# Kernel tuning notes

Measured on AMD Instinct MI355X. Metric: run time of the kernel, lower is better.

The kernel has to match this reference:

```python
import jax, jax.numpy as jnp
import numpy as np

L = 13   # num hidden states (embeddings + 12 layers)
B = 32   # batch
N = 512  # sequence length
H = 768  # per-layer hidden size
M = 384  # mapping_size = embed_size // downsample_D_factor
E = 768  # embed_size


def setup_inputs() -> dict:
    key = jax.random.key(0)
    ks = jax.random.split(key, 8)
    s = 0.02
    return {
        "all_hidden_features": jax.random.normal(ks[0], (L, B, N, H), jnp.float32),
        "lengths": jax.random.randint(ks[1], (B,), 1, N + 1),  # valid lengths in [1, N]
        "W_down": jax.random.normal(ks[2], (L, H, M), jnp.float32) * s,
        "b_down": jnp.zeros((L, M), jnp.float32),
        "g_down": jnp.ones((L, M), jnp.float32),
        "beta_down": jnp.zeros((L, M), jnp.float32),
        "W_proj": jax.random.normal(ks[3], (M, M), jnp.float32) * s,
        "b_proj": jnp.zeros((M,), jnp.float32),
        "g_proj": jnp.ones((M,), jnp.float32),
        "beta_proj": jnp.zeros((M,), jnp.float32),
        "W_up": jax.random.normal(ks[4], (M, E), jnp.float32) * s,
        "b_up": jnp.zeros((E,), jnp.float32),
        "W_gate": jax.random.normal(ks[5], (M, 1), jnp.float32) * s,
        "b_gate": jnp.zeros((1,), jnp.float32),
    }


def _ln(x, g, b, eps=1e-5):
    mu = jnp.mean(x, axis=-1, keepdims=True)
    var = jnp.var(x, axis=-1, keepdims=True)
    return (x - mu) * jax.lax.rsqrt(var + eps) * g + b


def reference(all_hidden_features, lengths, W_down, b_down, g_down, beta_down,
              W_proj, b_proj, g_proj, beta_proj, W_up, b_up, W_gate, b_gate):
    # mask: [B, N] 1.0 for valid positions
    mask = (jnp.arange(N)[None, :] < lengths[:, None]).astype(jnp.float32)

    # per-layer downsample: Linear + LayerNorm over all L layers at once -> [L, B, N, M]
    down = _ln(jnp.einsum('lbnh,lhm->lbnm', all_hidden_features, W_down)
               + b_down[:, None, None, :],
               g_down[:, None, None, :], beta_down[:, None, None, :])

    anchor_feat = down[-1]                      # [B, N, M]
    denom = jnp.sum(mask, axis=1)[:, None]      # [B, 1]
    anchor = jnp.sum(anchor_feat * mask[:, :, None], axis=1) / denom  # [B, M]

    targets = down[:-1]                         # [L-1, B, N, M]
    t_agg = jnp.sum(targets * mask[None, :, :, None], axis=2) / denom[None]  # [L-1, B, M]

    # cross-attention: relu + L1-normalized weights + identity, mask on context dim
    cw = jnp.einsum('bnm,lbkm->lbnk', anchor_feat, targets)  # [L-1, B, N, N]
    cw = jax.nn.relu(cw * mask[None, :, None, :])
    cw = cw / (jnp.sum(cw, axis=-1, keepdims=True) + 1e-8) + jnp.eye(N, dtype=cw.dtype)
    merged = jnp.einsum('lbnk,lbkm->lbnm', cw, targets)      # [L-1, B, N, M]

    # gated fusion across layers
    logits = (jnp.einsum('lbm,mo->lbo', anchor[None] * t_agg, W_gate) + b_gate)[..., 0]  # [L-1, B]
    conf = jax.nn.softmax(logits.T, axis=1)                  # [B, L-1]
    msum = jnp.einsum('lbnm,bl->bnm', merged, conf)          # [B, N, M]

    out = anchor_feat + _ln(msum @ W_proj + b_proj, g_proj, beta_proj)
    return (jax.nn.relu(out) @ W_up + b_up, lengths)
```

## Files before the change

kernel.cpp:

```cpp
#include <hip/hip_runtime.h>

#define LL 13
#define BB 32
#define NN 512
#define HH 768
#define MM 384
#define EE 768
#define BN (BB*NN)
#define K12 (12*NN)

typedef __attribute__((ext_vector_type(8))) short s16x8;
typedef __attribute__((ext_vector_type(4))) float f32x4;
typedef __attribute__((ext_vector_type(4))) unsigned int u32x4;
typedef unsigned int u32;
#define AS1 __attribute__((address_space(1)))
#define AS3 __attribute__((address_space(3)))

__device__ __forceinline__ u32 cvtpk2(float a, float b) {
    u32 r; asm("v_cvt_pk_bf16_f32 %0, %1, %2" : "=v"(r) : "v"(a), "v"(b));
    return r;
}
__device__ __forceinline__ short f2bf_hw(float f) {
    u32 r; asm("v_cvt_pk_bf16_f32 %0, %1, %2" : "=v"(r) : "v"(f), "v"(f));
    return (short)r;
}
__device__ __forceinline__ float bf2f(short h) {
    union { u32 u; float f; } c; c.u = ((u32)(unsigned short)h) << 16;
    return c.f;
}
__device__ __forceinline__ void gload16(const void* g, void* l) {
    __builtin_amdgcn_global_load_lds((const AS1 u32*)g, (AS3 u32*)l, 16, 0, 0);
}

template<int AM>
__device__ __forceinline__ void gemm_core(const char* At, const char* At2, int lda,
                                          const char* Bt, int ldb,
                                          int K, char* lds, f32x4 acc[4][4])
{
    const int tid  = threadIdx.x;
    const int lane = tid & 63;
    const int w    = tid >> 6;
    const int mt0 = (w >> 1) * 4;
    const int nt0 = (w & 1) * 4;

    const int rg0 = (w*2)*16 + (lane & 15);
    const int rg1 = rg0 + 16;
    const int kcb = (lane >> 4) * 16;
    const char* gb0 = Bt + (size_t)rg0 * ldb * 2 + kcb;
    const char* gb1 = Bt + (size_t)rg1 * ldb * 2 + kcb;
    const int lboff0 = 8192 + (w*2)*1024;
    const int lboff1 = lboff0 + 1024;

    auto mfma_step = [&](int bo) {
        s16x8 af[4], bf4[4];
        char* sA = lds + bo;
        char* sB = sA + 8192;
        #pragma unroll
        for (int i = 0; i < 4; ++i) af[i] = *(const s16x8*)(sA + ((mt0+i)<<10) + lane*16);
        #pragma unroll
        for (int j = 0; j < 4; ++j) bf4[j] = *(const s16x8*)(sB + ((nt0+j)<<10) + lane*16);
        #pragma unroll
        for (int i = 0; i < 4; ++i)
            #pragma unroll
            for (int j = 0; j < 4; ++j)
                acc[i][j] = __builtin_amdgcn_mfma_f32_16x16x32_bf16(af[i], bf4[j], acc[i][j], 0, 0, 0);
    };

    if (AM == 0) {
        const char* ga0 = At + (size_t)rg0 * lda * 2 + kcb;
        const char* ga1 = At + (size_t)rg1 * lda * 2 + kcb;
        const int laoff0 = (w*2)*1024, laoff1 = laoff0 + 1024;
        gload16(ga0, lds + laoff0); gload16(ga1, lds + laoff1);
        gload16(gb0, lds + lboff0); gload16(gb1, lds + lboff1);
        ga0 += 64; ga1 += 64; gb0 += 64; gb1 += 64;
        __syncthreads();
        int bo = 0;
        for (int k0 = 32; k0 < K; k0 += 32) {
            const int nbo = bo ^ 16384;
            gload16(ga0, lds + nbo + laoff0); gload16(ga1, lds + nbo + laoff1);
            gload16(gb0, lds + nbo + lboff0); gload16(gb1, lds + nbo + lboff1);
            ga0 += 64; ga1 += 64; gb0 += 64; gb1 += 64;
            mfma_step(bo);
            __syncthreads();
            bo = nbo;
        }
        mfma_step(bo);
    } else {
        size_t goff_[4]; int loff_[4];
        #pragma unroll
        for (int c = 0; c < 4; ++c) {
            int id = c*256 + tid;
            int row = id >> 3, c16 = id & 7;
            goff_[c] = (size_t)row * lda * 4 + c16 * 16;
            loff_[c] = ((row>>4)*64 + (row&15) + (c16>>1)*16)*16 + (c16&1)*8;
        }
        f32x4 g[4];
        #pragma unroll
        for (int c = 0; c < 4; ++c) {
            g[c] = *(const f32x4*)(At + goff_[c]);
            if (AM == 2) {
                f32x4 h = *(const f32x4*)(At2 + goff_[c]);
                g[c][0]+=h[0]; g[c][1]+=h[1]; g[c][2]+=h[2]; g[c][3]+=h[3];
            }
        }
        gload16(gb0, lds + lboff0); gload16(gb1, lds + lboff1);
        gb0 += 64; gb1 += 64;
        #pragma unroll
        for (int c = 0; c < 4; ++c) {
            u32* d = (u32*)(lds + loff_[c]);
            d[0] = cvtpk2(g[c][0], g[c][1]);
            d[1] = cvtpk2(g[c][2], g[c][3]);
        }
        __syncthreads();
        int bo = 0;
        size_t kb = 128;
        for (int k0 = 32; k0 < K; k0 += 32, kb += 128) {
            const int nbo = bo ^ 16384;
            #pragma unroll
            for (int c = 0; c < 4; ++c) {
                g[c] = *(const f32x4*)(At + goff_[c] + kb);
                if (AM == 2) {
                    f32x4 h = *(const f32x4*)(At2 + goff_[c] + kb);
                    g[c][0]+=h[0]; g[c][1]+=h[1]; g[c][2]+=h[2]; g[c][3]+=h[3];
                }
            }
            gload16(gb0, lds + nbo + lboff0); gload16(gb1, lds + nbo + lboff1);
            gb0 += 64; gb1 += 64;
            mfma_step(bo);
            #pragma unroll
            for (int c = 0; c < 4; ++c) {
                u32* d = (u32*)(lds + nbo + loff_[c]);
                d[0] = cvtpk2(g[c][0], g[c][1]);
                d[1] = cvtpk2(g[c][2], g[c][3]);
            }
            __syncthreads();
            bo = nbo;
        }
        mfma_step(bo);
    }
}

__device__ __forceinline__ void zero_acc(f32x4 acc[4][4]) {
    #pragma unroll
    for (int i = 0; i < 4; ++i)
        #pragma unroll
        for (int j = 0; j < 4; ++j) {
            acc[i][j][0] = 0.f; acc[i][j][1] = 0.f;
            acc[i][j][2] = 0.f; acc[i][j][3] = 0.f;
        }
}

__global__ __launch_bounds__(256) void k_zero(float* __restrict__ p, int n4)
{
    int i = blockIdx.x*256 + threadIdx.x;
    if (i < n4) { f32x4 z = {0.f,0.f,0.f,0.f}; ((f32x4*)p)[i] = z; }
}

__global__ __launch_bounds__(256) void k_wt(const float* __restrict__ in, short* __restrict__ out,
                                            int R, int C, size_t zin, size_t zout)
{
    __shared__ short L[64][80];
    const float* I = in + (size_t)blockIdx.z * zin;
    short* O = out + (size_t)blockIdx.z * zout;
    const int r0 = blockIdx.y * 64, c0 = blockIdx.x * 64;
    const int t = threadIdx.x;
    {
        int r = t >> 2, cq = (t & 3) * 16;
        const float* p = I + (size_t)(r0 + r) * C + c0 + cq;
        f32x4 u0 = *(const f32x4*)(p);
        f32x4 u1 = *(const f32x4*)(p + 4);
        f32x4 u2 = *(const f32x4*)(p + 8);
        f32x4 u3 = *(const f32x4*)(p + 12);
        u32x4 pa, pb;
        pa[0]=cvtpk2(u0[0],u0[1]); pa[1]=cvtpk2(u0[2],u0[3]);
        pa[2]=cvtpk2(u1[0],u1[1]); pa[3]=cvtpk2(u1[2],u1[3]);
        pb[0]=cvtpk2(u2[0],u2[1]); pb[1]=cvtpk2(u2[2],u2[3]);
        pb[2]=cvtpk2(u3[0],u3[1]); pb[3]=cvtpk2(u3[2],u3[3]);
        *(u32x4*)&L[r][cq]     = pa;
        *(u32x4*)&L[r][cq + 8] = pb;
    }
    __syncthreads();
    #pragma unroll
    for (int it = 0; it < 2; ++it) {
        int id = it * 256 + t;
        int cc = id >> 3, rq = id & 7;
        s16x8 v;
        #pragma unroll
        for (int e = 0; e < 8; ++e) v[e] = L[rq*8 + e][cc];
        *(s16x8*)(O + (size_t)(c0 + cc) * R + r0 + rq*8) = v;
    }
}

__global__ __launch_bounds__(256) void k_down(const float* __restrict__ X,
                                              const short* __restrict__ WdT,
                                              const float* __restrict__ bd,
                                              short* __restrict__ down)
{
    __shared__ char lds[36864];
    const int lg = ((blockIdx.x & 7) * 624) + (blockIdx.x >> 3);
    const int col0 = (lg % 3) * 128;
    const int row0 = ((lg / 3) & 127) * 128;
    const int l = lg / 384;
    const char* At = (const char*)(X   + (size_t)l*BN*HH + (size_t)row0*HH);
    const char* Bt = (const char*)(WdT + (size_t)l*MM*HH + (size_t)col0*HH);
    f32x4 acc[4][4]; zero_acc(acc);
    gemm_core<1>(At, nullptr, HH, Bt, HH, HH, lds, acc);

    const int tid = threadIdx.x, lane = tid & 63, w = tid >> 6;
    const int wr = w >> 1, wc = w & 1;
    float bj[4];
    #pragma unroll
    for (int j = 0; j < 4; ++j) bj[j] = bd[l*MM + col0 + wc*64 + j*16 + (lane & 15)];
    __syncthreads();
    short* ep = (short*)(lds + w * 9216);
    #pragma unroll
    for (int i = 0; i < 4; ++i) {
        int rr = i*16 + (lane >> 4) * 4;
        #pragma unroll
        for (int j = 0; j < 4; ++j) {
            int cc = j*16 + (lane & 15);
            #pragma unroll
            for (int r = 0; r < 4; ++r)
                ep[(rr + r)*72 + cc] = f2bf_hw(acc[i][j][r] + bj[j]);
        }
    }
    __syncthreads();
    short* C = down + (size_t)l*BN*MM;
    #pragma unroll
    for (int it = 0; it < 8; ++it) {
        int c = it*64 + lane;
        int row = c >> 3, kq = c & 7;
        s16x8 v = *(const s16x8*)(ep + row*72 + kq*8);
        int grow = row0 + wr*64 + row;
        int gcol = col0 + wc*64 + kq*8;
        *(s16x8*)(C + (size_t)grow*MM + gcol) = v;
    }
}

__global__ __launch_bounds__(256) void k_ln(short* __restrict__ down,
                                            const float* __restrict__ g,
                                            const float* __restrict__ beta,
                                            short* __restrict__ downTb,
                                            const int* __restrict__ lengths,
                                            float* __restrict__ t_raw,
                                            float* __restrict__ a_raw)
{
    __shared__ short Lt[64][392];
    __shared__ float sacc[4][384];
    const int blk = blockIdx.x;
    const int l = blk / (BB*8);
    const int rem = blk % (BB*8);
    const int b = rem >> 3;
    const int n0 = (rem & 7) * 64;
    const int tid = threadIdx.x, lane = tid & 63, w = tid >> 6;
    const int len = lengths[b];
    float racc[6] = {0.f,0.f,0.f,0.f,0.f,0.f};

    for (int it = 0; it < 16; ++it) {
        int ri = it*4 + w;
        int n = n0 + ri;
        short* p = down + (((size_t)l*BB + b)*NN + n) * MM;
        u32* pu = (u32*)p;
        float f[6]; float s = 0.f, s2 = 0.f;
        #pragma unroll
        for (int t = 0; t < 3; ++t) {
            u32 q = pu[lane + t*64];
            float lo = bf2f((short)(q & 0xffff));
            float hi = bf2f((short)(q >> 16));
            f[2*t] = lo; f[2*t+1] = hi;
            s += lo + hi; s2 += lo*lo + hi*hi;
        }
        #pragma unroll
        for (int off = 32; off; off >>= 1) { s += __shfl_xor(s, off); s2 += __shfl_xor(s2, off); }
        float mu  = s * (1.f/MM);
        float inv = rsqrtf(s2 * (1.f/MM) - mu*mu + 1e-5f);
        const bool valid = n < len;
        #pragma unroll
        for (int t = 0; t < 3; ++t) {
            int m0 = (lane + t*64) * 2;
            float o0 = (f[2*t]  -mu)*inv * g[l*MM + m0]     + beta[l*MM + m0];
            float o1 = (f[2*t+1]-mu)*inv * g[l*MM + m0 + 1] + beta[l*MM + m0 + 1];
            u32 pk = cvtpk2(o0, o1);
            pu[lane + t*64] = pk;
            ((u32*)&Lt[ri][0])[lane + t*64] = pk;
            if (valid) { racc[2*t] += o0; racc[2*t+1] += o1; }
        }
    }
    #pragma unroll
    for (int t = 0; t < 3; ++t) {
        int m0 = (lane + t*64) * 2;
        sacc[w][m0]     = racc[2*t];
        sacc[w][m0 + 1] = racc[2*t+1];
    }
    __syncthreads();
    if (w == 0) {
        float* dst = (l == 12) ? (a_raw + b*MM) : (t_raw + ((size_t)l*BB + b)*MM);
        #pragma unroll
        for (int t = 0; t < 3; ++t) {
            #pragma unroll
            for (int e = 0; e < 2; ++e) {
                int m = (lane + t*64)*2 + e;
                float tot = sacc[0][m] + sacc[1][m] + sacc[2][m] + sacc[3][m];
                atomicAdd(&dst[m], tot);
            }
        }
    }
    if (l == 12) return;
    short* O = downTb + ((size_t)b*MM*12 + l) * NN;
    #pragma unroll
    for (int it = 0; it < 12; ++it) {
        int id = it*256 + tid;
        int m = id >> 3, nq = id & 7;
        s16x8 vv;
        #pragma unroll
        for (int e = 0; e < 8; ++e) vv[e] = Lt[nq*8 + e][m];
        *(s16x8*)(O + (size_t)m*12*NN + n0 + nq*8) = vv;
    }
}

__global__ __launch_bounds__(64) void k_conf(const float* __restrict__ a_raw,
                                             const float* __restrict__ t_raw,
                                             const float* __restrict__ Wg,
                                             const float* __restrict__ bg,
                                             const int* __restrict__ lengths,
                                             float* __restrict__ conf)
{
    const int b = blockIdx.x;
    const int lane = threadIdx.x;
    const float len = (float)lengths[b];
    const float inv2 = 1.f/(len*len);
    float lg[12];
    #pragma unroll
    for (int l = 0; l < 12; ++l) {
        float s = 0.f;
        #pragma unroll
        for (int t = 0; t < 6; ++t) {
            int m = lane + t*64;
            s += a_raw[b*MM + m] * t_raw[((size_t)l*BB + b)*MM + m] * Wg[m];
        }
        #pragma unroll
        for (int off = 32; off; off >>= 1) s += __shfl_xor(s, off);
        lg[l] = s * inv2 + bg[0];
    }
    float mx = lg[0];
    #pragma unroll
    for (int l = 1; l < 12; ++l) mx = fmaxf(mx, lg[l]);
    float den = 0.f, e[12];
    #pragma unroll
    for (int l = 0; l < 12; ++l) { e[l] = expf(lg[l]-mx); den += e[l]; }
    if (lane == 0) {
        #pragma unroll
        for (int l = 0; l < 12; ++l) conf[b*12 + l] = e[l]/den;
    }
}

__global__ __launch_bounds__(512) void k_srow(const short* __restrict__ down,
                                              const int* __restrict__ lengths,
                                              const float* __restrict__ conf,
                                              short* __restrict__ cw)
{
    __shared__ char lds[81920];
    const int lg = ((blockIdx.x & 7) * 192) + (blockIdx.x >> 3);
    const int rowblk = lg & 3;
    const int z = lg >> 2;
    const int l = z % 12;
    const int b = z / 12;
    const int tid = threadIdx.x, lane = tid & 63, w = tid >> 6;
    const int wr = w >> 2, wcg = w & 3;

    const char* Ab = (const char*)(down + (((size_t)12*BB + b)*NN + rowblk*128)*MM);
    const char* Bb = (const char*)(down + ((size_t)l*BB + b)*NN*MM);

    const char* gp[5]; int lo[5];
    #pragma unroll
    for (int q = 0; q < 5; ++q) {
        int gidx = w*5 + q;
        const char* base = (gidx < 8) ? Ab : Bb;
        int grow = ((gidx < 8) ? gidx : (gidx - 8))*16 + (lane & 15);
        gp[q] = base + (size_t)grow * MM * 2 + (lane >> 4)*16;
        lo[q] = gidx*1024 + lane*16;
    }

    f32x4 acc[4][8];
    #pragma unroll
    for (int i = 0; i < 4; ++i)
        #pragma unroll
        for (int j = 0; j < 8; ++j) { acc[i][j][0]=0.f; acc[i][j][1]=0.f; acc[i][j][2]=0.f; acc[i][j][3]=0.f; }

    auto mfma_blk = [&](int bo) {
        s16x8 af[4], bf4[8];
        #pragma unroll
        for (int i = 0; i < 4; ++i) af[i] = *(const s16x8*)(lds + bo + ((wr*4 + i)<<10) + lane*16);
        #pragma unroll
        for (int j = 0; j < 8; ++j) bf4[j] = *(const s16x8*)(lds + bo + ((8 + wcg*8 + j)<<10) + lane*16);
        #pragma unroll
        for (int i = 0; i < 4; ++i)
            #pragma unroll
            for (int j = 0; j < 8; ++j)
                acc[i][j] = __builtin_amdgcn_mfma_f32_16x16x32_bf16(af[i], bf4[j], acc[i][j], 0, 0, 0);
    };

    #pragma unroll
    for (int q = 0; q < 5; ++q) { gload16(gp[q], lds + lo[q]); gp[q] += 64; }
    __syncthreads();
    int bo = 0;
    for (int t = 1; t < 12; ++t) {
        const int nbo = bo ^ 40960;
        #pragma unroll
        for (int q = 0; q < 5; ++q) { gload16(gp[q], lds + nbo + lo[q]); gp[q] += 64; }
        mfma_blk(bo);
        __syncthreads();
        bo = nbo;
    }
    mfma_blk(bo);

    const int len = lengths[b];
    const float cf = conf[b*12 + l];

    float ps[4][4];
    #pragma unroll
    for (int i = 0; i < 4; ++i)
        #pragma unroll
        for (int r = 0; r < 4; ++r) ps[i][r] = 0.f;
    #pragma unroll
    for (int i = 0; i < 4; ++i)
        #pragma unroll
        for (int j = 0; j < 8; ++j) {
            int c = wcg*128 + j*16 + (lane & 15);
            bool keep = c < len;
            #pragma unroll
            for (int r = 0; r < 4; ++r) {
                float v = keep ? fmaxf(acc[i][j][r], 0.f) : 0.f;
                acc[i][j][r] = v;
                ps[i][r] += v;
            }
        }
    #pragma unroll
    for (int off = 1; off < 16; off <<= 1)
        #pragma unroll
        for (int i = 0; i < 4; ++i)
            #pragma unroll
            for (int r = 0; r < 4; ++r) ps[i][r] += __shfl_xor(ps[i][r], off);
    float* rs = (float*)(lds + 73728);
    if ((lane & 15) == 0) {
        #pragma unroll
        for (int i = 0; i < 4; ++i)
            #pragma unroll
            for (int r = 0; r < 4; ++r)
                rs[wcg*128 + wr*64 + i*16 + (lane >> 4)*4 + r] = ps[i][r];
    }
    __syncthreads();
    float sc[4][4];
    #pragma unroll
    for (int i = 0; i < 4; ++i)
        #pragma unroll
        for (int r = 0; r < 4; ++r) {
            int row = wr*64 + i*16 + (lane >> 4)*4 + r;
            float tot = rs[row] + rs[128 + row] + rs[256 + row] + rs[384 + row];
            sc[i][r] = cf / (tot + 1e-8f);
        }
    short* ep = (short*)(lds + w * 9216);
    short* C = cw + ((size_t)b*NN + rowblk*128 + wr*64)*K12 + (size_t)l*NN + wcg*128;
    #pragma unroll
    for (int half = 0; half < 2; ++half) {
        #pragma unroll
        for (int i = 0; i < 4; ++i)
            #pragma unroll
            for (int jj = 0; jj < 4; ++jj) {
                int j = half*4 + jj;
                int cc = jj*16 + (lane & 15);
                int cg = wcg*128 + half*64 + cc;
                #pragma unroll
                for (int r = 0; r < 4; ++r) {
                    int rr = i*16 + (lane >> 4)*4 + r;
                    float o = acc[i][j][r] * sc[i][r];
                    int ng = rowblk*128 + wr*64 + rr;
                    if (ng == cg) o += cf;
                    ep[rr*72 + cc] = f2bf_hw(o);
                }
            }
        #pragma unroll
        for (int it = 0; it < 8; ++it) {
            int cdx = it*64 + lane;
            int row = cdx >> 3, kq = cdx & 7;
            s16x8 v = *(const s16x8*)(ep + row*72 + kq*8);
            *(s16x8*)(C + (size_t)row*K12 + half*64 + kq*8) = v;
        }
    }
}

__global__ __launch_bounds__(256) void k_merge(const short* __restrict__ cw,
                                               const short* __restrict__ downTb,
                                               float* __restrict__ msA,
                                               float* __restrict__ msB)
{
    __shared__ char lds[36864];
    const int lg = ((blockIdx.x & 7) * 96) + (blockIdx.x >> 3);
    const int col0 = (lg % 3) * 128;
    const int row0 = ((lg / 3) & 3) * 128;
    const int bkh = lg / 12;
    const int b  = bkh >> 1;
    const int kh = bkh & 1;
    const char* At = (const char*)(cw     + ((size_t)b*NN + row0)*K12 + kh*3072);
    const char* Bt = (const char*)(downTb + ((size_t)b*MM + col0)*K12 + kh*3072);
    f32x4 acc[4][4]; zero_acc(acc);
    gemm_core<0>(At, nullptr, K12, Bt, K12, 3072, lds, acc);

    const int tid = threadIdx.x, lane = tid & 63, w = tid >> 6;
    const int wr = w >> 1, wc = w & 1;
    float* msH = kh ? msB : msA;
    #pragma unroll
    for (int i = 0; i < 4; ++i)
        #pragma unroll
        for (int r = 0; r < 4; ++r) {
            int grow = row0 + wr*64 + i*16 + (lane >> 4)*4 + r;
            #pragma unroll
            for (int j = 0; j < 4; ++j) {
                int gcol = col0 + wc*64 + j*16 + (lane & 15);
                msH[((size_t)b*NN + grow)*MM + gcol] = acc[i][j][r];
            }
        }
}

__global__ __launch_bounds__(256) void k_proj(const float* __restrict__ msA,
                                              const float* __restrict__ msB,
                                              const short* __restrict__ WpT,
                                              const float* __restrict__ bp,
                                              float* __restrict__ tmp)
{
    __shared__ char lds[36864];
    const int lg = ((blockIdx.x & 7) * 48) + (blockIdx.x >> 3);
    const int col0 = (lg % 3) * 128;
    const int row0 = (lg / 3) * 128;
    const char* At  = (const char*)(msA + (size_t)row0*MM);
    const char* At2 = (const char*)(msB + (size_t)row0*MM);
    const char* Bt  = (const char*)(WpT + (size_t)col0*MM);
    f32x4 acc[4][4]; zero_acc(acc);
    gemm_core<2>(At, At2, MM, Bt, MM, MM, lds, acc);

    const int tid = threadIdx.x, lane = tid & 63, w = tid >> 6;
    const int wr = w >> 1, wc = w & 1;
    float bj[4];
    #pragma unroll
    for (int j = 0; j < 4; ++j) bj[j] = bp[col0 + wc*64 + j*16 + (lane & 15)];
    #pragma unroll
    for (int i = 0; i < 4; ++i)
        #pragma unroll
        for (int r = 0; r < 4; ++r) {
            int grow = row0 + wr*64 + i*16 + (lane >> 4)*4 + r;
            #pragma unroll
            for (int j = 0; j < 4; ++j) {
                int gcol = col0 + wc*64 + j*16 + (lane & 15);
                tmp[(size_t)grow*MM + gcol] = acc[i][j][r] + bj[j];
            }
        }
}

__global__ __launch_bounds__(256) void k_ln2(const float* __restrict__ tmp,
                                             const short* __restrict__ down,
                                             const float* __restrict__ g,
                                             const float* __restrict__ beta,
                                             short* __restrict__ R)
{
    const int row  = blockIdx.x*4 + (threadIdx.x >> 6);
    const int lane = threadIdx.x & 63;
    const float* p = tmp + (size_t)row*MM;
    const short* af = down + (size_t)12*BN*MM + (size_t)row*MM;
    float v[6]; float s = 0.f, s2 = 0.f;
    #pragma unroll
    for (int t = 0; t < 6; ++t) { v[t] = p[lane + t*64]; s += v[t]; s2 += v[t]*v[t]; }
    #pragma unroll
    for (int off = 32; off; off >>= 1) { s += __shfl_xor(s, off); s2 += __shfl_xor(s2, off); }
    float mu  = s * (1.f/MM);
    float inv = rsqrtf(s2 * (1.f/MM) - mu*mu + 1e-5f);
    #pragma unroll
    for (int t = 0; t < 6; ++t) {
        int m = lane + t*64;
        float o = bf2f(af[m]) + (v[t]-mu)*inv * g[m] + beta[m];
        R[(size_t)row*MM + m] = f2bf_hw(fmaxf(o, 0.f));
    }
}

__global__ __launch_bounds__(256) void k_up(const short* __restrict__ R,
                                            const short* __restrict__ WuT,
                                            const float* __restrict__ bu,
                                            float* __restrict__ Y)
{
    __shared__ char lds[32768];
    const int lg = ((blockIdx.x & 7) * 96) + (blockIdx.x >> 3);
    const int col0 = (lg % 6) * 128;
    const int row0 = (lg / 6) * 128;
    const char* At = (const char*)(R + (size_t)row0*MM);
    const char* Bt = (const char*)(WuT + (size_t)col0*MM);
    f32x4 acc[4][4]; zero_acc(acc);
    gemm_core<0>(At, nullptr, MM, Bt, MM, MM, lds, acc);

    const int tid = threadIdx.x, lane = tid & 63, w = tid >> 6;
    const int wr = w >> 1, wc = w & 1;
    float bj[4];
    #pragma unroll
    for (int j = 0; j < 4; ++j) bj[j] = bu[col0 + wc*64 + j*16 + (lane & 15)];
    #pragma unroll
    for (int i = 0; i < 4; ++i)
        #pragma unroll
        for (int r = 0; r < 4; ++r) {
            int grow = row0 + wr*64 + i*16 + (lane >> 4)*4 + r;
            #pragma unroll
            for (int j = 0; j < 4; ++j) {
                int gcol = col0 + wc*64 + j*16 + (lane & 15);
                Y[(size_t)grow*EE + gcol] = acc[i][j][r] + bj[j];
            }
        }
}

__global__ void k_len(const int* __restrict__ lengths, float* __restrict__ out)
{
    if (threadIdx.x < BB)
        out[(size_t)BB*NN*EE + threadIdx.x] = (float)lengths[threadIdx.x];
}

extern "C" void kernel_launch(void* const* d_in, const int* in_sizes, int n_in,
                              void* d_out, int out_size, void* d_ws, size_t ws_size,
                              hipStream_t stream)
{
    const float* X    = (const float*)d_in[0];
    const int*   len  = (const int*)  d_in[1];
    const float* Wd   = (const float*)d_in[2];
    const float* bd   = (const float*)d_in[3];
    const float* gd   = (const float*)d_in[4];
    const float* betd = (const float*)d_in[5];
    const float* Wp   = (const float*)d_in[6];
    const float* bp   = (const float*)d_in[7];
    const float* gp   = (const float*)d_in[8];
    const float* betp = (const float*)d_in[9];
    const float* Wu   = (const float*)d_in[10];
    const float* bu   = (const float*)d_in[11];
    const float* Wg   = (const float*)d_in[12];
    const float* bg   = (const float*)d_in[13];
    float* out = (float*)d_out;

    float* ws     = (float*)d_ws;
    float* tmp    = ws;
    float* t_raw  = tmp + 6291456;
    float* a_raw  = t_raw + 147456;
    float* conf   = a_raw + 12288;
    short* down   = (short*)(conf + 384);
    short* downTb = down   + (size_t)81788928;
    short* cw     = downTb + (size_t)75497472;
    short* R      = cw     + (size_t)100663296;
    short* WdT    = R      + (size_t)6291456;
    short* WpT    = WdT    + (size_t)3833856;
    short* WuT    = WpT    + (size_t)147456;
    float* msA    = (float*)(WuT + 294912);
    float* msB    = msA + 6291456;

    k_zero<<<156, 256, 0, stream>>>(t_raw, (147456+12288)/4);
    k_wt<<<dim3(6, 12, 13), 256, 0, stream>>>(Wd, WdT, HH, MM, (size_t)HH*MM, (size_t)HH*MM);
    k_wt<<<dim3(6, 6, 1),   256, 0, stream>>>(Wp, WpT, MM, MM, 0, 0);
    k_wt<<<dim3(12, 6, 1),  256, 0, stream>>>(Wu, WuT, MM, EE, 0, 0);
    k_down<<<4992, 256, 0, stream>>>(X, WdT, bd, down);
    k_ln<<<LL*BB*8, 256, 0, stream>>>(down, gd, betd, downTb, len, t_raw, a_raw);
    k_conf<<<BB, 64, 0, stream>>>(a_raw, t_raw, Wg, bg, len, conf);
    k_srow<<<1536, 512, 0, stream>>>(down, len, conf, cw);
    k_merge<<<768, 256, 0, stream>>>(cw, downTb, msA, msB);
    k_proj<<<384, 256, 0, stream>>>(msA, msB, WpT, bp, tmp);
    k_ln2<<<BN/4, 256, 0, stream>>>(tmp, down, gp, betp, R);
    k_up<<<768, 256, 0, stream>>>(R, WuT, bu, out);
    k_len<<<1, 64, 0, stream>>>(len, out);
}
```

Measured before the change: 899.8 us.

## Triple-buffer bf16 GEMM core with vmcnt-based barriers; fold length write into k_conf

The bf16 GEMM path (AM==0) moves from double to triple buffering in LDS. It keeps two global-to-LDS loads in flight and replaces __syncthreads with explicit s_waitcnt vmcnt(4) plus s_barrier, so the next tile's load overlaps the MFMA work. The fp32-A path (AM==1) is unrolled by two with ping-pong register staging, so global loads of one tile overlap the conversion and compute of another. The separate k_len launch is removed and its write moved into k_conf. In exchange, LDS use per block rises to 48KB in k_merge and k_up, which may lower occupancy, and the hand-written waitcnt counts must be exactly right.

```diff
diff --git a/kernel.cpp b/kernel.cpp
--- a/kernel.cpp
+++ b/kernel.cpp
@@ -32,6 +32,11 @@
     __builtin_amdgcn_global_load_lds((const AS1 u32*)g, (AS3 u32*)l, 16, 0, 0);
 }
 
+#define CBAR(N) do { \
+    asm volatile("s_waitcnt vmcnt(" #N ") lgkmcnt(0)\n\ts_barrier" ::: "memory"); \
+    __builtin_amdgcn_sched_barrier(0); \
+} while (0)
+
 template<int AM>
 __device__ __forceinline__ void gemm_core(const char* At, const char* At2, int lda,
                                           const char* Bt, int ldb,
@@ -70,22 +75,29 @@
         const char* ga0 = At + (size_t)rg0 * lda * 2 + kcb;
         const char* ga1 = At + (size_t)rg1 * lda * 2 + kcb;
         const int laoff0 = (w*2)*1024, laoff1 = laoff0 + 1024;
+        const int nsteps = K >> 5;
         gload16(ga0, lds + laoff0); gload16(ga1, lds + laoff1);
         gload16(gb0, lds + lboff0); gload16(gb1, lds + lboff1);
         ga0 += 64; ga1 += 64; gb0 += 64; gb1 += 64;
-        __syncthreads();
+        gload16(ga0, lds + 16384 + laoff0); gload16(ga1, lds + 16384 + laoff1);
+        gload16(gb0, lds + 16384 + lboff0); gload16(gb1, lds + 16384 + lboff1);
+        ga0 += 64; ga1 += 64; gb0 += 64; gb1 += 64;
+        CBAR(4);
         int bo = 0;
-        for (int k0 = 32; k0 < K; k0 += 32) {
-            const int nbo = bo ^ 16384;
-            gload16(ga0, lds + nbo + laoff0); gload16(ga1, lds + nbo + laoff1);
-            gload16(gb0, lds + nbo + lboff0); gload16(gb1, lds + nbo + lboff1);
+        for (int t = 0; t < nsteps - 2; ++t) {
+            int so = bo + 32768; if (so >= 49152) so -= 49152;
+            gload16(ga0, lds + so + laoff0); gload16(ga1, lds + so + laoff1);
+            gload16(gb0, lds + so + lboff0); gload16(gb1, lds + so + lboff1);
             ga0 += 64; ga1 += 64; gb0 += 64; gb1 += 64;
             mfma_step(bo);
-            __syncthreads();
-            bo = nbo;
+            CBAR(4);
+            bo += 16384; if (bo == 49152) bo = 0;
         }
         mfma_step(bo);
-    } else {
+        CBAR(0);
+        bo += 16384; if (bo == 49152) bo = 0;
+        mfma_step(bo);
+    } else if (AM == 1) {
         size_t goff_[4]; int loff_[4];
         #pragma unroll
         for (int c = 0; c < 4; ++c) {
@@ -94,14 +106,71 @@
             goff_[c] = (size_t)row * lda * 4 + c16 * 16;
             loff_[c] = ((row>>4)*64 + (row&15) + (c16>>1)*16)*16 + (c16&1)*8;
         }
+        const int nsteps = K >> 5;
+        f32x4 gA[4], gB[4];
+        gload16(gb0, lds + lboff0); gload16(gb1, lds + lboff1); gb0 += 64; gb1 += 64;
+        #pragma unroll
+        for (int c = 0; c < 4; ++c) gA[c] = *(const f32x4*)(At + goff_[c]);
+        #pragma unroll
+        for (int c = 0; c < 4; ++c) {
+            u32* d = (u32*)(lds + loff_[c]);
+            d[0] = cvtpk2(gA[c][0], gA[c][1]); d[1] = cvtpk2(gA[c][2], gA[c][3]);
+        }
+        #pragma unroll
+        for (int c = 0; c < 4; ++c) gA[c] = *(const f32x4*)(At + goff_[c] + 128);
+        CBAR(4);
+        int bo = 0;
+        size_t kb = 256;
+        for (int t = 0; t < nsteps - 2; t += 2, kb += 256) {
+            const int nbo = bo ^ 16384;
+            gload16(gb0, lds + nbo + lboff0); gload16(gb1, lds + nbo + lboff1); gb0 += 64; gb1 += 64;
+            #pragma unroll
+            for (int c = 0; c < 4; ++c) gB[c] = *(const f32x4*)(At + goff_[c] + kb);
+            #pragma unroll
+            for (int c = 0; c < 4; ++c) {
+                u32* d = (u32*)(lds + nbo + loff_[c]);
+                d[0] = cvtpk2(gA[c][0], gA[c][1]); d[1] = cvtpk2(gA[c][2], gA[c][3]);
+            }
+            mfma_step(bo);
+            CBAR(4);
+            gload16(gb0, lds + bo + lboff0); gload16(gb1, lds + bo + lboff1); gb0 += 64; gb1 += 64;
+            #pragma unroll
+            for (int c = 0; c < 4; ++c) gA[c] = *(const f32x4*)(At + goff_[c] + kb + 128);
+            #pragma unroll
+            for (int c = 0; c < 4; ++c) {
+                u32* d = (u32*)(lds + bo + loff_[c]);
+                d[0] = cvtpk2(gB[c][0], gB[c][1]); d[1] = cvtpk2(gB[c][2], gB[c][3]);
+            }
+            mfma_step(nbo);
+            CBAR(4);
+        }
+        {
+            const int nbo = bo ^ 16384;
+            gload16(gb0, lds + nbo + lboff0); gload16(gb1, lds + nbo + lboff1);
+            #pragma unroll
+            for (int c = 0; c < 4; ++c) {
+                u32* d = (u32*)(lds + nbo + loff_[c]);
+                d[0] = cvtpk2(gA[c][0], gA[c][1]); d[1] = cvtpk2(gA[c][2], gA[c][3]);
+            }
+            mfma_step(bo);
+            CBAR(0);
+            mfma_step(nbo);
+        }
+    } else {
+        size_t goff_[4]; int loff_[4];
+        #pragma unroll
+        for (int c = 0; c < 4; ++c) {
+            int id = c*256 + tid;
+            int row = id >> 3, c16 = id & 7;
+            goff_[c] = (size_t)row * lda * 4 + c16 * 16;
+            loff_[c] = ((row>>4)*64 + (row&15) + (c16>>1)*16)*16 + (c16&1)*8;
+        }
         f32x4 g[4];
         #pragma unroll
         for (int c = 0; c < 4; ++c) {
             g[c] = *(const f32x4*)(At + goff_[c]);
-            if (AM == 2) {
-                f32x4 h = *(const f32x4*)(At2 + goff_[c]);
-                g[c][0]+=h[0]; g[c][1]+=h[1]; g[c][2]+=h[2]; g[c][3]+=h[3];
-            }
+            f32x4 h = *(const f32x4*)(At2 + goff_[c]);
+            g[c][0]+=h[0]; g[c][1]+=h[1]; g[c][2]+=h[2]; g[c][3]+=h[3];
         }
         gload16(gb0, lds + lboff0); gload16(gb1, lds + lboff1);
         gb0 += 64; gb1 += 64;
@@ -119,10 +188,8 @@
             #pragma unroll
             for (int c = 0; c < 4; ++c) {
                 g[c] = *(const f32x4*)(At + goff_[c] + kb);
-                if (AM == 2) {
-                    f32x4 h = *(const f32x4*)(At2 + goff_[c] + kb);
-                    g[c][0]+=h[0]; g[c][1]+=h[1]; g[c][2]+=h[2]; g[c][3]+=h[3];
-                }
+                f32x4 h = *(const f32x4*)(At2 + goff_[c] + kb);
+                g[c][0]+=h[0]; g[c][1]+=h[1]; g[c][2]+=h[2]; g[c][3]+=h[3];
             }
             gload16(gb0, lds + nbo + lboff0); gload16(gb1, lds + nbo + lboff1);
             gb0 += 64; gb1 += 64;
@@ -323,7 +390,8 @@
                                              const float* __restrict__ Wg,
                                              const float* __restrict__ bg,
                                              const int* __restrict__ lengths,
-                                             float* __restrict__ conf)
+                                             float* __restrict__ conf,
+                                             float* __restrict__ out)
 {
     const int b = blockIdx.x;
     const int lane = threadIdx.x;
@@ -351,6 +419,7 @@
     if (lane == 0) {
         #pragma unroll
         for (int l = 0; l < 12; ++l) conf[b*12 + l] = e[l]/den;
+        out[(size_t)BB*NN*EE + b] = len;
     }
 }
 
@@ -494,7 +563,7 @@
                                                float* __restrict__ msA,
                                                float* __restrict__ msB)
 {
-    __shared__ char lds[36864];
+    __shared__ char lds[49152];
     const int lg = ((blockIdx.x & 7) * 96) + (blockIdx.x >> 3);
     const int col0 = (lg % 3) * 128;
     const int row0 = ((lg / 3) & 3) * 128;
@@ -586,7 +655,7 @@
                                             const float* __restrict__ bu,
                                             float* __restrict__ Y)
 {
-    __shared__ char lds[32768];
+    __shared__ char lds[49152];
     const int lg = ((blockIdx.x & 7) * 96) + (blockIdx.x >> 3);
     const int col0 = (lg % 6) * 128;
     const int row0 = (lg / 6) * 128;
@@ -611,12 +680,6 @@
                 Y[(size_t)grow*EE + gcol] = acc[i][j][r] + bj[j];
             }
         }
-}
-
-__global__ void k_len(const int* __restrict__ lengths, float* __restrict__ out)
-{
-    if (threadIdx.x < BB)
-        out[(size_t)BB*NN*EE + threadIdx.x] = (float)lengths[threadIdx.x];
 }
 
 extern "C" void kernel_launch(void* const* d_in, const int* in_sizes, int n_in,
@@ -660,11 +723,10 @@
     k_wt<<<dim3(12, 6, 1),  256, 0, stream>>>(Wu, WuT, MM, EE, 0, 0);
     k_down<<<4992, 256, 0, stream>>>(X, WdT, bd, down);
     k_ln<<<LL*BB*8, 256, 0, stream>>>(down, gd, betd, downTb, len, t_raw, a_raw);
-    k_conf<<<BB, 64, 0, stream>>>(a_raw, t_raw, Wg, bg, len, conf);
+    k_conf<<<BB, 64, 0, stream>>>(a_raw, t_raw, Wg, bg, len, conf, out);
     k_srow<<<1536, 512, 0, stream>>>(down, len, conf, cw);
     k_merge<<<768, 256, 0, stream>>>(cw, downTb, msA, msB);
     k_proj<<<384, 256, 0, stream>>>(msA, msB, WpT, bp, tmp);
     k_ln2<<<BN/4, 256, 0, stream>>>(tmp, down, gp, betp, R);
     k_up<<<768, 256, 0, stream>>>(R, WuT, bu, out);
-    k_len<<<1, 64, 0, stream>>>(len, out);
-}
+}
```

New measurement: 927.6 us. 3.1% more time.

## Widen k_down tiles to full 384 columns per block, fold length output into k_conf

Applied to the files above, without the earlier changes.

k_down now uses 512-thread blocks that each compute a 128x384 tile covering the whole mapping dimension. Each fp32 activation row is therefore read and converted to bf16 once instead of three times, cutting global traffic on the largest GEMM. The price is double the LDS (72 KB), 24 accumulator tiles per wave with higher register pressure, and a two-pass epilogue. The lengths output write moves into k_conf, removing one launch. The AM==2 guard in the shared gemm_core is also dropped, so AM==1 instantiations would read a null At2, but k_down no longer calls gemm_core<1>.

```diff
diff --git a/kernel.cpp b/kernel.cpp
--- a/kernel.cpp
+++ b/kernel.cpp
@@ -98,10 +98,8 @@
         #pragma unroll
         for (int c = 0; c < 4; ++c) {
             g[c] = *(const f32x4*)(At + goff_[c]);
-            if (AM == 2) {
-                f32x4 h = *(const f32x4*)(At2 + goff_[c]);
-                g[c][0]+=h[0]; g[c][1]+=h[1]; g[c][2]+=h[2]; g[c][3]+=h[3];
-            }
+            f32x4 h = *(const f32x4*)(At2 + goff_[c]);
+            g[c][0]+=h[0]; g[c][1]+=h[1]; g[c][2]+=h[2]; g[c][3]+=h[3];
         }
         gload16(gb0, lds + lboff0); gload16(gb1, lds + lboff1);
         gb0 += 64; gb1 += 64;
@@ -119,10 +117,8 @@
             #pragma unroll
             for (int c = 0; c < 4; ++c) {
                 g[c] = *(const f32x4*)(At + goff_[c] + kb);
-                if (AM == 2) {
-                    f32x4 h = *(const f32x4*)(At2 + goff_[c] + kb);
-                    g[c][0]+=h[0]; g[c][1]+=h[1]; g[c][2]+=h[2]; g[c][3]+=h[3];
-                }
+                f32x4 h = *(const f32x4*)(At2 + goff_[c] + kb);
+                g[c][0]+=h[0]; g[c][1]+=h[1]; g[c][2]+=h[2]; g[c][3]+=h[3];
             }
             gload16(gb0, lds + nbo + lboff0); gload16(gb1, lds + nbo + lboff1);
             gb0 += 64; gb1 += 64;
@@ -191,28 +187,94 @@
     }
 }
 
-__global__ __launch_bounds__(256) void k_down(const float* __restrict__ X,
+__global__ __launch_bounds__(512) void k_down(const float* __restrict__ X,
                                               const short* __restrict__ WdT,
                                               const float* __restrict__ bd,
                                               short* __restrict__ down)
 {
-    __shared__ char lds[36864];
-    const int lg = ((blockIdx.x & 7) * 624) + (blockIdx.x >> 3);
-    const int col0 = (lg % 3) * 128;
-    const int row0 = ((lg / 3) & 127) * 128;
-    const int l = lg / 384;
-    const char* At = (const char*)(X   + (size_t)l*BN*HH + (size_t)row0*HH);
-    const char* Bt = (const char*)(WdT + (size_t)l*MM*HH + (size_t)col0*HH);
-    f32x4 acc[4][4]; zero_acc(acc);
-    gemm_core<1>(At, nullptr, HH, Bt, HH, HH, lds, acc);
-
+    __shared__ char lds[73728];
+    const int lg = ((blockIdx.x & 7) * 208) + (blockIdx.x >> 3);
+    const int rowtile = lg & 127;
+    const int l = lg >> 7;
     const int tid = threadIdx.x, lane = tid & 63, w = tid >> 6;
-    const int wr = w >> 1, wc = w & 1;
-    float bj[4];
-    #pragma unroll
-    for (int j = 0; j < 4; ++j) bj[j] = bd[l*MM + col0 + wc*64 + j*16 + (lane & 15)];
+    const int wr = w >> 2, wcg = w & 3;
+
+    const char* Ab = (const char*)(X + ((size_t)l*BN + rowtile*128)*HH);
+    const char* Bb = (const char*)(WdT + (size_t)l*MM*HH);
+
+    const char* gp[3]; int lo[3];
+    #pragma unroll
+    for (int q = 0; q < 3; ++q) {
+        int gidx = w*3 + q;
+        gp[q] = Bb + (size_t)(gidx*16 + (lane & 15)) * HH * 2 + (lane >> 4)*16;
+        lo[q] = 8192 + gidx*1024 + lane*16;
+    }
+    size_t goff_[2]; int loff_[2];
+    #pragma unroll
+    for (int c = 0; c < 2; ++c) {
+        int id = c*512 + tid;
+        int row = id >> 3, c16 = id & 7;
+        goff_[c] = (size_t)row * HH * 4 + c16 * 16;
+        loff_[c] = ((row>>4)*64 + (row&15) + (c16>>1)*16)*16 + (c16&1)*8;
+    }
+
+    f32x4 acc[4][6];
+    #pragma unroll
+    for (int i = 0; i < 4; ++i)
+        #pragma unroll
+        for (int j = 0; j < 6; ++j) { acc[i][j][0]=0.f; acc[i][j][1]=0.f; acc[i][j][2]=0.f; acc[i][j][3]=0.f; }
+
+    auto mfma_step = [&](int bo) {
+        s16x8 af[4], bf4[6];
+        #pragma unroll
+        for (int i = 0; i < 4; ++i) af[i] = *(const s16x8*)(lds + bo + ((wr*4 + i)<<10) + lane*16);
+        #pragma unroll
+        for (int j = 0; j < 6; ++j) bf4[j] = *(const s16x8*)(lds + bo + 8192 + ((wcg*6 + j)<<10) + lane*16);
+        #pragma unroll
+        for (int i = 0; i < 4; ++i)
+            #pragma unroll
+            for (int j = 0; j < 6; ++j)
+                acc[i][j] = __builtin_amdgcn_mfma_f32_16x16x32_bf16(af[i], bf4[j], acc[i][j], 0, 0, 0);
+    };
+
+    f32x4 gA[2];
+    #pragma unroll
+    for (int c = 0; c < 2; ++c) gA[c] = *(const f32x4*)(Ab + goff_[c]);
+    #pragma unroll
+    for (int q = 0; q < 3; ++q) { gload16(gp[q], lds + lo[q]); gp[q] += 64; }
+    #pragma unroll
+    for (int c = 0; c < 2; ++c) {
+        u32* d = (u32*)(lds + loff_[c]);
+        d[0] = cvtpk2(gA[c][0], gA[c][1]);
+        d[1] = cvtpk2(gA[c][2], gA[c][3]);
+    }
+    __syncthreads();
+    int bo = 0;
+    size_t kb = 128;
+    for (int k0 = 32; k0 < HH; k0 += 32, kb += 128) {
+        const int nbo = bo ^ 32768;
+        #pragma unroll
+        for (int c = 0; c < 2; ++c) gA[c] = *(const f32x4*)(Ab + goff_[c] + kb);
+        #pragma unroll
+        for (int q = 0; q < 3; ++q) { gload16(gp[q], lds + nbo + lo[q]); gp[q] += 64; }
+        mfma_step(bo);
+        #pragma unroll
+        for (int c = 0; c < 2; ++c) {
+            u32* d = (u32*)(lds + nbo + loff_[c]);
+            d[0] = cvtpk2(gA[c][0], gA[c][1]);
+            d[1] = cvtpk2(gA[c][2], gA[c][3]);
+        }
+        __syncthreads();
+        bo = nbo;
+    }
+    mfma_step(bo);
+
+    float bj[6];
+    #pragma unroll
+    for (int j = 0; j < 6; ++j) bj[j] = bd[l*MM + wcg*96 + j*16 + (lane & 15)];
     __syncthreads();
     short* ep = (short*)(lds + w * 9216);
+    short* C = down + ((size_t)l*BN + rowtile*128 + wr*64)*MM + wcg*96;
     #pragma unroll
     for (int i = 0; i < 4; ++i) {
         int rr = i*16 + (lane >> 4) * 4;
@@ -225,15 +287,32 @@
         }
     }
     __syncthreads();
-    short* C = down + (size_t)l*BN*MM;
     #pragma unroll
     for (int it = 0; it < 8; ++it) {
-        int c = it*64 + lane;
-        int row = c >> 3, kq = c & 7;
+        int cdx = it*64 + lane;
+        int row = cdx >> 3, kq = cdx & 7;
         s16x8 v = *(const s16x8*)(ep + row*72 + kq*8);
-        int grow = row0 + wr*64 + row;
-        int gcol = col0 + wc*64 + kq*8;
-        *(s16x8*)(C + (size_t)grow*MM + gcol) = v;
+        *(s16x8*)(C + (size_t)row*MM + kq*8) = v;
+    }
+    __syncthreads();
+    #pragma unroll
+    for (int i = 0; i < 4; ++i) {
+        int rr = i*16 + (lane >> 4) * 4;
+        #pragma unroll
+        for (int j = 4; j < 6; ++j) {
+            int cc = (j-4)*16 + (lane & 15);
+            #pragma unroll
+            for (int r = 0; r < 4; ++r)
+                ep[(rr + r)*40 + cc] = f2bf_hw(acc[i][j][r] + bj[j]);
+        }
+    }
+    __syncthreads();
+    #pragma unroll
+    for (int it = 0; it < 4; ++it) {
+        int cdx = it*64 + lane;
+        int row = cdx >> 2, kq = cdx & 3;
+        s16x8 v = *(const s16x8*)(ep + row*40 + kq*8);
+        *(s16x8*)(C + (size_t)row*MM + 64 + kq*8) = v;
     }
 }
 
@@ -323,7 +402,8 @@
                                              const float* __restrict__ Wg,
                                              const float* __restrict__ bg,
                                              const int* __restrict__ lengths,
-                                             float* __restrict__ conf)
+                                             float* __restrict__ conf,
+                                             float* __restrict__ out)
 {
     const int b = blockIdx.x;
     const int lane = threadIdx.x;
@@ -351,6 +431,7 @@
     if (lane == 0) {
         #pragma unroll
         for (int l = 0; l < 12; ++l) conf[b*12 + l] = e[l]/den;
+        out[(size_t)BB*NN*EE + b] = len;
     }
 }
 
@@ -611,12 +692,6 @@
                 Y[(size_t)grow*EE + gcol] = acc[i][j][r] + bj[j];
             }
         }
-}
-
-__global__ void k_len(const int* __restrict__ lengths, float* __restrict__ out)
-{
-    if (threadIdx.x < BB)
-        out[(size_t)BB*NN*EE + threadIdx.x] = (float)lengths[threadIdx.x];
 }
 
 extern "C" void kernel_launch(void* const* d_in, const int* in_sizes, int n_in,
@@ -658,13 +733,12 @@
     k_wt<<<dim3(6, 12, 13), 256, 0, stream>>>(Wd, WdT, HH, MM, (size_t)HH*MM, (size_t)HH*MM);
     k_wt<<<dim3(6, 6, 1),   256, 0, stream>>>(Wp, WpT, MM, MM, 0, 0);
     k_wt<<<dim3(12, 6, 1),  256, 0, stream>>>(Wu, WuT, MM, EE, 0, 0);
-    k_down<<<4992, 256, 0, stream>>>(X, WdT, bd, down);
+    k_down<<<1664, 512, 0, stream>>>(X, WdT, bd, down);
     k_ln<<<LL*BB*8, 256, 0, stream>>>(down, gd, betd, downTb, len, t_raw, a_raw);
-    k_conf<<<BB, 64, 0, stream>>>(a_raw, t_raw, Wg, bg, len, conf);
+    k_conf<<<BB, 64, 0, stream>>>(a_raw, t_raw, Wg, bg, len, conf, out);
     k_srow<<<1536, 512, 0, stream>>>(down, len, conf, cw);
     k_merge<<<768, 256, 0, stream>>>(cw, downTb, msA, msB);
     k_proj<<<384, 256, 0, stream>>>(msA, msB, WpT, bp, tmp);
     k_ln2<<<BN/4, 256, 0, stream>>>(tmp, down, gp, betp, R);
     k_up<<<768, 256, 0, stream>>>(R, WuT, bu, out);
-    k_len<<<1, 64, 0, stream>>>(len, out);
-}
+}
```

After: 945.2 us. +5.0%, slower.
